# Optimization experiments

Hardware: AMD Instinct MI355X
Metric: run time of the kernel (lower is better)

Reference implementation:

```python
import jax, jax.numpy as jnp
import numpy as np

N_NODES = 100000
N_EDGES = 1000000
D_IN = 64
D_HID = 64
D_OUT = 64


def setup_inputs() -> dict:
    key = jax.random.key(0)
    ks = jax.random.split(key, 8)
    x = jax.random.normal(ks[0], (N_NODES, D_IN), dtype=jnp.float32)
    edge_index = jax.random.randint(ks[1], (2, N_EDGES), 0, N_NODES, dtype=jnp.int64)
    s = 1.0 / np.sqrt(D_IN)
    # SAGEConv layer 1: lin_l (applied to aggregated neighbors, with bias), lin_r (root, no bias)
    W1l = jax.random.uniform(ks[2], (D_HID, D_IN), jnp.float32, -s, s)
    b1l = jnp.zeros((D_HID,), jnp.float32)
    W1r = jax.random.uniform(ks[3], (D_HID, D_IN), jnp.float32, -s, s)
    s2 = 1.0 / np.sqrt(D_HID)
    W2l = jax.random.uniform(ks[4], (D_OUT, D_HID), jnp.float32, -s2, s2)
    b2l = jnp.zeros((D_OUT,), jnp.float32)
    W2r = jax.random.uniform(ks[5], (D_OUT, D_HID), jnp.float32, -s2, s2)
    return {"x": x, "edge_index": edge_index,
            "W1l": W1l, "b1l": b1l, "W1r": W1r,
            "W2l": W2l, "b2l": b2l, "W2r": W2r}


def _sage_conv(x, src, dst, Wl, bl, Wr):
    # mean-aggregate neighbor features (messages flow src -> dst)
    msg_sum = jax.ops.segment_sum(x[src], dst, num_segments=N_NODES)  # [N, d]
    deg = jax.ops.segment_sum(jnp.ones((src.shape[0],), x.dtype), dst, num_segments=N_NODES)
    agg = msg_sum / jnp.maximum(deg, 1.0)[:, None]
    return agg @ Wl.T + bl + x @ Wr.T


def reference(x, edge_index, W1l, b1l, W1r, W2l, b2l, W2r):
    src, dst = edge_index[0], edge_index[1]
    h = _sage_conv(x, src, dst, W1l, b1l, W1r)
    h = jax.nn.relu(h)
    # dropout is identity in eval mode
    out = _sage_conv(h, src, dst, W2l, b2l, W2r)
    return out
```

## Files before the change

kernel.cpp:

```cpp
#include <hip/hip_runtime.h>

#define D 64
#define BK_SHIFT 8
#define BK_MASK 255
#define SEGCAP 4096
#define ESLICE 4096

typedef __attribute__((ext_vector_type(8))) short short8;
typedef __attribute__((ext_vector_type(4))) float floatx4;

__device__ __forceinline__ ushort f2bf(float f) {
    unsigned u = __float_as_uint(f);
    u += 0x7fffu + ((u >> 16) & 1u);
    return (ushort)(u >> 16);
}
__device__ __forceinline__ float bf2f(ushort h) {
    return __int_as_float(((unsigned)h) << 16);
}

__global__ void cast_bkcount_kernel(const float* __restrict__ x, ushort* __restrict__ xh,
                                    const int* __restrict__ ei, int* __restrict__ bkcnt,
                                    int* __restrict__ scnt,
                                    int n4, int E, int B, int castb) {
    int bid = blockIdx.x;
    int tid = threadIdx.x;
    if (bid < castb) {
        int i = bid * 256 + tid;
        if (i >= n4) return;
        float4 v = ((const float4*)x)[i];
        ushort4 r;
        r.x = f2bf(v.x); r.y = f2bf(v.y); r.z = f2bf(v.z); r.w = f2bf(v.w);
        ((ushort4*)xh)[i] = r;
        return;
    }
    __shared__ int h[512];
    h[tid] = 0; h[tid + 256] = 0;
    __syncthreads();
    int slice = bid - castb;
    int e0 = slice * ESLICE;
#pragma unroll 4
    for (int it = 0; it < ESLICE / 256; ++it) {
        int e = e0 + it * 256 + tid;
        if (e < E) atomicAdd(&h[ei[E + e] >> BK_SHIFT], 1);
    }
    __syncthreads();
    scnt[slice * 512 + tid] = h[tid];
    scnt[slice * 512 + 256 + tid] = h[tid + 256];
    if (tid < B && h[tid]) atomicAdd(&bkcnt[tid], h[tid]);
    int t2 = tid + 256;
    if (t2 < B && h[t2]) atomicAdd(&bkcnt[t2], h[t2]);
}

__global__ void bkscan_kernel(const int* __restrict__ bkcnt, int* __restrict__ bkbeg,
                              int* __restrict__ bkcur, int B) {
    __shared__ int wsum[8];
    int tid = threadIdx.x;
    int lane = tid & 63, w = tid >> 6;
    int c = (tid < B) ? bkcnt[tid] : 0;
    int p = c;
#pragma unroll
    for (int o = 1; o < 64; o <<= 1) {
        int u = __shfl_up(p, o, 64);
        if (lane >= o) p += u;
    }
    if (lane == 63) wsum[w] = p;
    __syncthreads();
    int base = 0;
    for (int ww = 0; ww < w; ++ww) base += wsum[ww];
    int excl = base + p - c;
    if (tid < B) { bkbeg[tid] = excl; bkcur[tid] = excl; }
    if (tid == B - 1) bkbeg[B] = excl + c;
}

__global__ void route_kernel(const int* __restrict__ ei, const int* __restrict__ scnt,
                             int* __restrict__ bkcur, int* __restrict__ bucketed,
                             int E, int B) {
    __shared__ int h[512];
    __shared__ int gb[512];
    int tid = threadIdx.x;
    int slice = blockIdx.x;
    int c0 = scnt[slice * 512 + tid];
    int c1 = scnt[slice * 512 + 256 + tid];
    gb[tid] = c0 ? atomicAdd(&bkcur[tid], c0) : 0;
    gb[tid + 256] = c1 ? atomicAdd(&bkcur[tid + 256], c1) : 0;
    h[tid] = 0; h[tid + 256] = 0;
    __syncthreads();
    int e0 = slice * ESLICE;
#pragma unroll 4
    for (int it = 0; it < ESLICE / 256; ++it) {
        int e = e0 + it * 256 + tid;
        if (e < E) {
            int dst = ei[E + e];
            int key = dst >> BK_SHIFT;
            int src = ei[e];
            int r = atomicAdd(&h[key], 1);
            bucketed[gb[key] + r] = (src << BK_SHIFT) | (dst & BK_MASK);
        }
    }
}

__global__ void csr_kernel(const int* __restrict__ bucketed, const int* __restrict__ bkbeg,
                           int* __restrict__ srclist, int* __restrict__ beg,
                           int* __restrict__ cnt, int* __restrict__ hist, int N) {
    __shared__ int lcnt[256];
    __shared__ int lbeg[256];
    __shared__ int seg[SEGCAP];
    __shared__ int wsum[4];
    __shared__ int lh[64];
    int k = blockIdx.x;
    int tid = threadIdx.x;
    int nd0 = k << BK_SHIFT;
    int nn = min(256, N - nd0);
    int ebeg = bkbeg[k], eend = bkbeg[k + 1];
    int ecnt = eend - ebeg;
    lcnt[tid] = 0;
    if (tid < 64) lh[tid] = 0;
    __syncthreads();
    for (int e = ebeg + tid; e < eend; e += 256)
        atomicAdd(&lcnt[bucketed[e] & BK_MASK], 1);
    __syncthreads();
    int c = lcnt[tid];
    int lane = tid & 63, w = tid >> 6;
    int p = c;
#pragma unroll
    for (int o = 1; o < 64; o <<= 1) {
        int u = __shfl_up(p, o, 64);
        if (lane >= o) p += u;
    }
    if (lane == 63) wsum[w] = p;
    __syncthreads();
    int base = 0;
    for (int ww = 0; ww < w; ++ww) base += wsum[ww];
    int excl = base + p - c;
    lbeg[tid] = excl;
    lcnt[tid] = 0;
    __syncthreads();
    if (ecnt <= SEGCAP) {
        for (int e = ebeg + tid; e < eend; e += 256) {
            int v = bucketed[e];
            int key = v & BK_MASK;
            int pos = lbeg[key] + atomicAdd(&lcnt[key], 1);
            seg[pos] = v >> BK_SHIFT;
        }
        __syncthreads();
        for (int i = tid; i < ecnt; i += 256)
            srclist[ebeg + i] = seg[i];
    } else {
        for (int e = ebeg + tid; e < eend; e += 256) {
            int v = bucketed[e];
            int key = v & BK_MASK;
            int pos = lbeg[key] + atomicAdd(&lcnt[key], 1);
            srclist[ebeg + pos] = v >> BK_SHIFT;
        }
    }
    __syncthreads();
    if (tid < nn) {
        int dg = lcnt[tid];
        cnt[nd0 + tid] = dg;
        beg[nd0 + tid] = ebeg + lbeg[tid];
        atomicAdd(&lh[dg < 63 ? dg : 63], 1);
    }
    __syncthreads();
    if (tid < 64 && lh[tid]) atomicAdd(&hist[tid], lh[tid]);
}

__global__ void scatter_kernel(const int* __restrict__ cnt, const int* __restrict__ hist,
                               int* __restrict__ bincur0, int* __restrict__ perm, int N) {
    __shared__ int lh[64];
    __shared__ int lbase[64];
    __shared__ int sbase[64];
    int tid = threadIdx.x;
    if (tid < 64) {
        lh[tid] = 0;
        int c = hist[tid];
        int p = c;
#pragma unroll
        for (int o = 1; o < 64; o <<= 1) {
            int u = __shfl_up(p, o, 64);
            if (tid >= o) p += u;
        }
        sbase[tid] = N - p;
    }
    __syncthreads();
    int i = blockIdx.x * blockDim.x + tid;
    int bin = 0, slot = 0;
    if (i < N) {
        int c = cnt[i];
        bin = c < 63 ? c : 63;
        slot = atomicAdd(&lh[bin], 1);
    }
    __syncthreads();
    if (tid < 64 && lh[tid] > 0) lbase[tid] = sbase[tid] + atomicAdd(&bincur0[tid], lh[tid]);
    __syncthreads();
    if (i < N) perm[lbase[bin] + slot] = i;
}


__global__ void __launch_bounds__(256, 3) sage_kernel(
    const ushort* __restrict__ inh,
    const int* __restrict__ perm,
    const int* __restrict__ beg_, const int* __restrict__ cnt_,
    const int* __restrict__ srclist,
    const float* __restrict__ Wl, const float* __restrict__ bl,
    const float* __restrict__ Wr,
    float* __restrict__ out_f32,
    ushort* __restrict__ out_bf,
    int N, int relu) {
    __shared__ short8 fL[8][64];
    __shared__ short8 fR[8][64];
    __shared__ float ot[4][16 * 68];
    int tid = threadIdx.x;
    int lane = tid & 63;
    {
        int c = tid >> 6;
        int n = lane & 15;
        int q = lane >> 4;
#pragma unroll
        for (int s = 0; s < 2; ++s) {
            const float* pl = Wl + (c * 16 + n) * D + s * 32 + q * 8;
            const float* pr = Wr + (c * 16 + n) * D + s * 32 + q * 8;
            short8 vl, vr;
#pragma unroll
            for (int j = 0; j < 8; ++j) {
                vl[j] = (short)f2bf(pl[j]);
                vr[j] = (short)f2bf(pr[j]);
            }
            fL[c * 2 + s][lane] = vl;
            fR[c * 2 + s][lane] = vr;
        }
    }
    __syncthreads();

    int m = lane & 15;
    int q = lane >> 4;
    float* otw = &ot[tid >> 6][0];
    float b0 = bl[m], b1 = bl[16 + m], b2 = bl[32 + m], b3 = bl[48 + m];
    int gwave   = blockIdx.x * 4 + (tid >> 6);
    int nwaves  = gridDim.x * 4;
    int ngroups = (N + 15) >> 4;

    for (int g = gwave; g < ngroups; g += nwaves) {
        int base = g * 16;
        bool nv = (base + m) < N;
        int node = nv ? perm[base + m] : 0;
        int beg = nv ? beg_[node] : 0;
        int deg = nv ? cnt_[node] : 0;

        int md = deg;
        md = max(md, __shfl_xor(md, 1, 64));
        md = max(md, __shfl_xor(md, 2, 64));
        md = max(md, __shfl_xor(md, 4, 64));
        md = max(md, __shfl_xor(md, 8, 64));

        float f0[8], f1[8];
#pragma unroll
        for (int u = 0; u < 8; ++u) { f0[u] = 0.f; f1[u] = 0.f; }

        for (int j = 0; j < md; j += 4) {
            int si0, si1, si2, si3;
            {
                int j0 = j,     i0 = beg + ((j0 < deg) ? j0 : 0);
                int j1 = j + 1, i1 = beg + ((j1 < deg) ? j1 : 0);
                int j2 = j + 2, i2 = beg + ((j2 < deg) ? j2 : 0);
                int j3 = j + 3, i3 = beg + ((j3 < deg) ? j3 : 0);
                si0 = srclist[i0]; si1 = srclist[i1];
                si2 = srclist[i2]; si3 = srclist[i3];
            }
            const ushort* rp0 = inh + (size_t)si0 * D;
            const ushort* rp1 = inh + (size_t)si1 * D;
            const ushort* rp2 = inh + (size_t)si2 * D;
            const ushort* rp3 = inh + (size_t)si3 * D;
            short8 lo0 = *(const short8*)(rp0 + q * 8);
            short8 hi0 = *(const short8*)(rp0 + 32 + q * 8);
            short8 lo1 = *(const short8*)(rp1 + q * 8);
            short8 hi1 = *(const short8*)(rp1 + 32 + q * 8);
            short8 lo2 = *(const short8*)(rp2 + q * 8);
            short8 hi2 = *(const short8*)(rp2 + 32 + q * 8);
            short8 lo3 = *(const short8*)(rp3 + q * 8);
            short8 hi3 = *(const short8*)(rp3 + 32 + q * 8);
            float m0 = (j     < deg) ? 1.f : 0.f;
            float m1 = (j + 1 < deg) ? 1.f : 0.f;
            float m2 = (j + 2 < deg) ? 1.f : 0.f;
            float m3 = (j + 3 < deg) ? 1.f : 0.f;
#pragma unroll
            for (int u = 0; u < 8; ++u) {
                f0[u] = fmaf(m0, bf2f((ushort)lo0[u]), f0[u]);
                f1[u] = fmaf(m0, bf2f((ushort)hi0[u]), f1[u]);
                f0[u] = fmaf(m1, bf2f((ushort)lo1[u]), f0[u]);
                f1[u] = fmaf(m1, bf2f((ushort)hi1[u]), f1[u]);
                f0[u] = fmaf(m2, bf2f((ushort)lo2[u]), f0[u]);
                f1[u] = fmaf(m2, bf2f((ushort)hi2[u]), f1[u]);
                f0[u] = fmaf(m3, bf2f((ushort)lo3[u]), f0[u]);
                f1[u] = fmaf(m3, bf2f((ushort)hi3[u]), f1[u]);
            }
        }

        float scale = (deg > 0) ? 1.0f / (float)deg : 0.0f;
        short8 a0, a1;
#pragma unroll
        for (int u = 0; u < 8; ++u) {
            a0[u] = (short)f2bf(f0[u] * scale);
            a1[u] = (short)f2bf(f1[u] * scale);
        }

        const ushort* rr = inh + (size_t)node * D;
        short8 r0 = *(const short8*)(rr + q * 8);
        short8 r1 = *(const short8*)(rr + 32 + q * 8);

#pragma unroll
        for (int c = 0; c < 4; ++c) {
            float bc = (c == 0) ? b0 : (c == 1) ? b1 : (c == 2) ? b2 : b3;
            floatx4 acc = {bc, bc, bc, bc};
            acc = __builtin_amdgcn_mfma_f32_16x16x32_bf16(a0, fL[c * 2 + 0][lane], acc, 0, 0, 0);
            acc = __builtin_amdgcn_mfma_f32_16x16x32_bf16(a1, fL[c * 2 + 1][lane], acc, 0, 0, 0);
            acc = __builtin_amdgcn_mfma_f32_16x16x32_bf16(r0, fR[c * 2 + 0][lane], acc, 0, 0, 0);
            acc = __builtin_amdgcn_mfma_f32_16x16x32_bf16(r1, fR[c * 2 + 1][lane], acc, 0, 0, 0);
#pragma unroll
            for (int r = 0; r < 4; ++r) {
                float v = acc[r];
                if (relu) v = fmaxf(v, 0.f);
                otw[(q * 4 + r) * 68 + c * 16 + m] = v;
            }
        }

        int rho = lane >> 2;
        int q4  = lane & 3;
        int onode = __shfl(node, rho, 64);
        const float* sp = &otw[rho * 68 + q4 * 16];
        if (base + rho < N) {
            if (out_bf) {
                uint u[8];
#pragma unroll
                for (int j = 0; j < 8; ++j)
                    u[j] = (uint)f2bf(sp[2 * j]) | ((uint)f2bf(sp[2 * j + 1]) << 16);
                uint4* dp = (uint4*)(out_bf + (size_t)onode * D + q4 * 16);
                uint4 w0 = {u[0], u[1], u[2], u[3]};
                uint4 w1 = {u[4], u[5], u[6], u[7]};
                dp[0] = w0; dp[1] = w1;
            } else {
                float4* dp = (float4*)(out_f32 + (size_t)onode * D + q4 * 16);
                const float4* s4 = (const float4*)sp;
                dp[0] = s4[0]; dp[1] = s4[1]; dp[2] = s4[2]; dp[3] = s4[3];
            }
        }
    }
}

extern "C" void kernel_launch(void* const* d_in, const int* in_sizes, int n_in,
                              void* d_out, int out_size, void* d_ws, size_t ws_size,
                              hipStream_t stream) {
    const float* x   = (const float*)d_in[0];
    const int*   ei  = (const int*)d_in[1];
    const float* W1l = (const float*)d_in[2];
    const float* b1l = (const float*)d_in[3];
    const float* W1r = (const float*)d_in[4];
    const float* W2l = (const float*)d_in[5];
    const float* b2l = (const float*)d_in[6];
    const float* W2r = (const float*)d_in[7];
    float* out = (float*)d_out;

    int N = in_sizes[0] / D;
    int E = in_sizes[1] / 2;
    int B = (N + BK_MASK) >> BK_SHIFT;
    int eslices = (E + ESLICE - 1) / ESLICE;

    char* ws = (char*)d_ws;
    ushort* xh = (ushort*)ws;
    ushort* hh = xh + (size_t)N * D;
    int*   bucketed = (int*)hh;
    int*   srclist  = (int*)(ws + (size_t)2 * N * D * 2);
    int*   beg      = srclist + E + 64;
    int*   cnt      = beg + N;
    int*   perm     = cnt + N;
    int*   hist     = perm + N;
    int*   bincur0  = hist + 64;
    int*   bkcnt    = bincur0 + 64;
    int*   bkbeg    = bkcnt + 512;
    int*   bkcur    = bkbeg + 513;
    int*   scnt     = bkcur + 512;

    (void)hipMemsetAsync(hist, 0, (64 + 64 + 512) * sizeof(int), stream);

    int n4 = N * D / 4;
    int castb = (n4 + 255) / 256;
    cast_bkcount_kernel<<<castb + eslices, 256, 0, stream>>>(x, xh, ei, bkcnt, scnt,
                                                             n4, E, B, castb);
    bkscan_kernel<<<1, 512, 0, stream>>>(bkcnt, bkbeg, bkcur, B);
    route_kernel<<<eslices, 256, 0, stream>>>(ei, scnt, bkcur, bucketed, E, B);
    csr_kernel<<<B, 256, 0, stream>>>(bucketed, bkbeg, srclist, beg, cnt, hist, N);
    int nblocks = (N + 255) / 256;
    scatter_kernel<<<nblocks, 256, 0, stream>>>(cnt, hist, bincur0, perm, N);

    int ngroups = (N + 15) / 16;
    int sblocks = (ngroups + 3) / 4;
    sage_kernel<<<sblocks, 256, 0, stream>>>(xh, perm, beg, cnt, srclist,
                                             W1l, b1l, W1r, nullptr, hh, N, 1);
    sage_kernel<<<sblocks, 256, 0, stream>>>(hh, perm, beg, cnt, srclist,
                                             W2l, b2l, W2r, out, nullptr, N, 0);
}
```

Baseline: 217.5 us.

## Fuse bucket scan into route kernel and write SAGE outputs directly from MFMA

Drops the single-block bucket scan launch. Each route block now recomputes the prefix scan of bucket counts redundantly and takes per-slice offsets by atomics on a zeroed offset array. In the SAGE kernel, the LDS transpose staging buffer is removed, and each lane writes its MFMA accumulator elements straight to global memory as scalar stores. Launch bounds rise to 5 blocks per CU for higher occupancy. The trade-off is many narrow uncoalesced 2- or 4-byte scattered stores instead of 16-byte vector stores.

```diff
diff --git a/kernel.cpp b/kernel.cpp
--- a/kernel.cpp
+++ b/kernel.cpp
@@ -51,13 +51,20 @@
     if (t2 < B && h[t2]) atomicAdd(&bkcnt[t2], h[t2]);
 }
 
-__global__ void bkscan_kernel(const int* __restrict__ bkcnt, int* __restrict__ bkbeg,
-                              int* __restrict__ bkcur, int B) {
-    __shared__ int wsum[8];
-    int tid = threadIdx.x;
+__global__ void route_kernel(const int* __restrict__ ei, const int* __restrict__ scnt,
+                             const int* __restrict__ bkcnt, int* __restrict__ bkoff,
+                             int* __restrict__ bkbeg, int* __restrict__ bucketed,
+                             int E, int B) {
+    __shared__ int h[512];
+    __shared__ int gb[512];
+    __shared__ int wsum[4];
+    int tid = threadIdx.x;
+    int slice = blockIdx.x;
+    int a = (2 * tid < B) ? bkcnt[2 * tid] : 0;
+    int b = (2 * tid + 1 < B) ? bkcnt[2 * tid + 1] : 0;
+    int s = a + b;
     int lane = tid & 63, w = tid >> 6;
-    int c = (tid < B) ? bkcnt[tid] : 0;
-    int p = c;
+    int p = s;
 #pragma unroll
     for (int o = 1; o < 64; o <<= 1) {
         int u = __shfl_up(p, o, 64);
@@ -67,22 +74,19 @@
     __syncthreads();
     int base = 0;
     for (int ww = 0; ww < w; ++ww) base += wsum[ww];
-    int excl = base + p - c;
-    if (tid < B) { bkbeg[tid] = excl; bkcur[tid] = excl; }
-    if (tid == B - 1) bkbeg[B] = excl + c;
-}
-
-__global__ void route_kernel(const int* __restrict__ ei, const int* __restrict__ scnt,
-                             int* __restrict__ bkcur, int* __restrict__ bucketed,
-                             int E, int B) {
-    __shared__ int h[512];
-    __shared__ int gb[512];
-    int tid = threadIdx.x;
-    int slice = blockIdx.x;
+    int excl = base + p - s;
+    gb[2 * tid] = excl;
+    gb[2 * tid + 1] = excl + a;
+    if (slice == 0) {
+        bkbeg[2 * tid] = excl;
+        bkbeg[2 * tid + 1] = excl + a;
+        if (tid == 255) bkbeg[512] = excl + s;
+    }
+    __syncthreads();
     int c0 = scnt[slice * 512 + tid];
     int c1 = scnt[slice * 512 + 256 + tid];
-    gb[tid] = c0 ? atomicAdd(&bkcur[tid], c0) : 0;
-    gb[tid + 256] = c1 ? atomicAdd(&bkcur[tid + 256], c1) : 0;
+    if (c0) gb[tid] += atomicAdd(&bkoff[tid], c0);
+    if (c1) gb[tid + 256] += atomicAdd(&bkoff[tid + 256], c1);
     h[tid] = 0; h[tid + 256] = 0;
     __syncthreads();
     int e0 = slice * ESLICE;
@@ -196,7 +200,7 @@
 }
 
 
-__global__ void __launch_bounds__(256, 3) sage_kernel(
+__global__ void __launch_bounds__(256, 5) sage_kernel(
     const ushort* __restrict__ inh,
     const int* __restrict__ perm,
     const int* __restrict__ beg_, const int* __restrict__ cnt_,
@@ -208,7 +212,6 @@
     int N, int relu) {
     __shared__ short8 fL[8][64];
     __shared__ short8 fR[8][64];
-    __shared__ float ot[4][16 * 68];
     int tid = threadIdx.x;
     int lane = tid & 63;
     {
@@ -233,7 +236,6 @@
 
     int m = lane & 15;
     int q = lane >> 4;
-    float* otw = &ot[tid >> 6][0];
     float b0 = bl[m], b1 = bl[16 + m], b2 = bl[32 + m], b3 = bl[48 + m];
     int gwave   = blockIdx.x * 4 + (tid >> 6);
     int nwaves  = gridDim.x * 4;
@@ -307,6 +309,15 @@
         short8 r0 = *(const short8*)(rr + q * 8);
         short8 r1 = *(const short8*)(rr + 32 + q * 8);
 
+        int on0 = __shfl(node, q * 4 + 0, 64);
+        int on1 = __shfl(node, q * 4 + 1, 64);
+        int on2 = __shfl(node, q * 4 + 2, 64);
+        int on3 = __shfl(node, q * 4 + 3, 64);
+        bool v0 = (base + q * 4 + 0) < N;
+        bool v1 = (base + q * 4 + 1) < N;
+        bool v2 = (base + q * 4 + 2) < N;
+        bool v3 = (base + q * 4 + 3) < N;
+
 #pragma unroll
         for (int c = 0; c < 4; ++c) {
             float bc = (c == 0) ? b0 : (c == 1) ? b1 : (c == 2) ? b2 : b3;
@@ -319,28 +330,13 @@
             for (int r = 0; r < 4; ++r) {
                 float v = acc[r];
                 if (relu) v = fmaxf(v, 0.f);
-                otw[(q * 4 + r) * 68 + c * 16 + m] = v;
-            }
-        }
-
-        int rho = lane >> 2;
-        int q4  = lane & 3;
-        int onode = __shfl(node, rho, 64);
-        const float* sp = &otw[rho * 68 + q4 * 16];
-        if (base + rho < N) {
-            if (out_bf) {
-                uint u[8];
-#pragma unroll
-                for (int j = 0; j < 8; ++j)
-                    u[j] = (uint)f2bf(sp[2 * j]) | ((uint)f2bf(sp[2 * j + 1]) << 16);
-                uint4* dp = (uint4*)(out_bf + (size_t)onode * D + q4 * 16);
-                uint4 w0 = {u[0], u[1], u[2], u[3]};
-                uint4 w1 = {u[4], u[5], u[6], u[7]};
-                dp[0] = w0; dp[1] = w1;
-            } else {
-                float4* dp = (float4*)(out_f32 + (size_t)onode * D + q4 * 16);
-                const float4* s4 = (const float4*)sp;
-                dp[0] = s4[0]; dp[1] = s4[1]; dp[2] = s4[2]; dp[3] = s4[3];
+                int onr = (r == 0) ? on0 : (r == 1) ? on1 : (r == 2) ? on2 : on3;
+                bool vr = (r == 0) ? v0 : (r == 1) ? v1 : (r == 2) ? v2 : v3;
+                if (vr) {
+                    size_t off = (size_t)onr * D + c * 16 + m;
+                    if (out_bf) out_bf[off] = f2bf(v);
+                    else        out_f32[off] = v;
+                }
             }
         }
     }
@@ -375,18 +371,18 @@
     int*   hist     = perm + N;
     int*   bincur0  = hist + 64;
     int*   bkcnt    = bincur0 + 64;
-    int*   bkbeg    = bkcnt + 512;
-    int*   bkcur    = bkbeg + 513;
-    int*   scnt     = bkcur + 512;
-
-    (void)hipMemsetAsync(hist, 0, (64 + 64 + 512) * sizeof(int), stream);
+    int*   bkoff    = bkcnt + 512;
+    int*   bkbeg    = bkoff + 512;
+    int*   scnt     = bkbeg + 513;
+
+    (void)hipMemsetAsync(hist, 0, (64 + 64 + 512 + 512) * sizeof(int), stream);
 
     int n4 = N * D / 4;
     int castb = (n4 + 255) / 256;
     cast_bkcount_kernel<<<castb + eslices, 256, 0, stream>>>(x, xh, ei, bkcnt, scnt,
                                                              n4, E, B, castb);
-    bkscan_kernel<<<1, 512, 0, stream>>>(bkcnt, bkbeg, bkcur, B);
-    route_kernel<<<eslices, 256, 0, stream>>>(ei, scnt, bkcur, bucketed, E, B);
+    route_kernel<<<eslices, 256, 0, stream>>>(ei, scnt, bkcnt, bkoff, bkbeg,
+                                              bucketed, E, B);
     csr_kernel<<<B, 256, 0, stream>>>(bucketed, bkbeg, srclist, beg, cnt, hist, N);
     int nblocks = (N + 255) / 256;
     scatter_kernel<<<nblocks, 256, 0, stream>>>(cnt, hist, bincur0, perm, N);
```

Result: slower. 277.6 us (+27.6%).
